# Kernel optimization log

Hardware: AMD Instinct MI355X
Metric: run time of the kernel (lower is better)

## Reference

```python
import jax, jax.numpy as jnp
import numpy as np

N_NODES = 50000
N_FEAT = 128
N_HIDDEN = 256
N_CLASSES = 1
N_EDGES = 800000


def gcn_layer(x, src, dst, W, b, n_nodes):
    """GCNConv: D^-1/2 (A + I) D^-1/2 X W + b, via gather-scatter over edges."""
    h = x @ W  # [N, out]
    # add self loops
    loop = jnp.arange(n_nodes, dtype=src.dtype)
    s = jnp.concatenate([src, loop])
    d = jnp.concatenate([dst, loop])
    deg = jax.ops.segment_sum(jnp.ones_like(d, dtype=h.dtype), d, num_segments=n_nodes)
    inv_sqrt = jax.lax.rsqrt(jnp.maximum(deg, 1.0))
    norm = inv_sqrt[s] * inv_sqrt[d]  # [E+N]
    msgs = h[s] * norm[:, None]       # gather: [E+N, out]
    out = jax.ops.segment_sum(msgs, d, num_segments=n_nodes)  # scatter-add
    return out + b


def setup_inputs() -> dict:
    key = jax.random.key(0)
    k1, k2, k3, k4 = jax.random.split(key, 4)
    x = jax.random.normal(k1, (N_NODES, N_FEAT), dtype=jnp.float32)
    edge_index = jax.random.randint(k2, (2, N_EDGES), 0, N_NODES, dtype=jnp.int32)
    s1 = 1.0 / np.sqrt(N_FEAT)
    s2 = 1.0 / np.sqrt(N_HIDDEN)
    W1 = jax.random.uniform(k3, (N_FEAT, N_HIDDEN), jnp.float32, -s1, s1)
    b1 = jnp.zeros((N_HIDDEN,), jnp.float32)
    W2 = jax.random.uniform(k4, (N_HIDDEN, N_CLASSES), jnp.float32, -s2, s2)
    b2 = jnp.zeros((N_CLASSES,), jnp.float32)
    return {"x": x, "edge_index": edge_index, "W1": W1, "b1": b1, "W2": W2, "b2": b2}


def reference(x, edge_index, W1, b1, W2, b2):
    src, dst = edge_index[0], edge_index[1]
    n = x.shape[0]
    h = gcn_layer(x, src, dst, W1, b1, n)
    h = jax.nn.relu(h)  # dropout=0.0 -> identity
    out = gcn_layer(h, src, dst, W2, b2, n)
    return out  # [N, n_classes]
```

## Files before the change

kernel.cpp:

```cpp
#include <hip/hip_runtime.h>

typedef unsigned int uint;
typedef unsigned short ushort;
typedef __attribute__((ext_vector_type(8))) short short8;
typedef __attribute__((ext_vector_type(4))) float f32x4;

#define CAP  64
#define BM16 16
#define STR  68

__device__ __forceinline__ float bf_lo(uint p) { return __uint_as_float(p << 16); }
__device__ __forceinline__ float bf_hi(uint p) { return __uint_as_float(p & 0xffff0000u); }
__device__ __forceinline__ uint rne_lo(uint u) { return (u + 0x7fffu + ((u >> 16) & 1u)) >> 16; }
__device__ __forceinline__ uint rne_hi(uint u) { return (u + 0x7fffu + ((u >> 16) & 1u)) & 0xffff0000u; }

__global__ void k_bucket(const int* __restrict__ src, const int* __restrict__ dst,
                         int* __restrict__ cnt, ushort* __restrict__ col,
                         const float* __restrict__ W1, uint* __restrict__ wpack, int E) {
  int gid = blockIdx.x * blockDim.x + threadIdx.x;
  if (gid < 4096) {
    int kk = gid >> 10, rem = gid & 1023, ntile = rem >> 6, lane = rem & 63;
    int quad = lane >> 4, nn = ntile * 16 + (lane & 15);
    uint d[4];
#pragma unroll
    for (int jp = 0; jp < 4; ++jp) {
      int k = kk * 32 + quad * 8 + 2 * jp;
      uint lo = rne_lo(__float_as_uint(W1[k * 256 + nn]));
      uint hi = rne_hi(__float_as_uint(W1[(k + 1) * 256 + nn]));
      d[jp] = lo | hi;
    }
    *(uint4*)&wpack[gid * 4] = make_uint4(d[0], d[1], d[2], d[3]);
  } else {
    int e = gid - 4096;
    if (e < E) {
      int d = dst[e];
      int s = src[e];
      int p = atomicAdd(&cnt[d], 1);
      if (p < CAP) col[d * CAP + p] = (ushort)s;
    }
  }
}

__global__ void k_prep2(const float2* __restrict__ x2, const int* __restrict__ cnt,
                        uint* __restrict__ xs, float* __restrict__ inv,
                        int N, int nconv) {
  int gid = blockIdx.x * blockDim.x + threadIdx.x;
  if (gid < N) {
    inv[gid] = rsqrtf((float)(cnt[gid] + 1));
  } else if (gid < N + nconv) {
    int cid = gid - N;
    int node = cid >> 6;
    float invd = rsqrtf((float)(cnt[node] + 1));
    float2 f = x2[cid];
    xs[cid] = rne_lo(__float_as_uint(invd * f.x)) | rne_hi(__float_as_uint(invd * f.y));
  }
}

__global__ __launch_bounds__(256, 2) void k_agg_gemm(
    const uint* __restrict__ xs, const ushort* __restrict__ col,
    const int* __restrict__ cnt, const float* __restrict__ inv,
    const uint* __restrict__ wpack, const float* __restrict__ b1,
    const float* __restrict__ W2, float* __restrict__ cz, int N) {
  __shared__ uint As[BM16 * STR];
  __shared__ float red[64];
  int t = threadIdx.x, wave = t >> 6, lane = t & 63;
  int m0 = blockIdx.x * BM16;

  for (int rr = 0; rr < 4; ++rr) {
    int m = wave * 4 + rr;
    int node = m0 + m;
    float2 acc = make_float2(0.f, 0.f);
    if (node < N) {
      uint pd = xs[(size_t)node * 64 + lane];
      acc.x = bf_lo(pd);
      acc.y = bf_hi(pd);
      int e = min(cnt[node], CAP);
      int ce = (int)col[node * CAP + lane];
      int p = 0;
      for (; p + 15 < e; p += 16) {
        uint pv[16];
#pragma unroll
        for (int j = 0; j < 16; ++j) {
          int s = __shfl(ce, p + j);
          pv[j] = xs[(size_t)s * 64 + lane];
        }
#pragma unroll
        for (int j = 0; j < 16; ++j) {
          acc.x += bf_lo(pv[j]);
          acc.y += bf_hi(pv[j]);
        }
      }
      for (; p + 3 < e; p += 4) {
        uint pv[4];
#pragma unroll
        for (int j = 0; j < 4; ++j) {
          int s = __shfl(ce, p + j);
          pv[j] = xs[(size_t)s * 64 + lane];
        }
#pragma unroll
        for (int j = 0; j < 4; ++j) {
          acc.x += bf_lo(pv[j]);
          acc.y += bf_hi(pv[j]);
        }
      }
      for (; p < e; ++p) {
        int s = __shfl(ce, p);
        uint p0 = xs[(size_t)s * 64 + lane];
        acc.x += bf_lo(p0);
        acc.y += bf_hi(p0);
      }
      float invd = inv[node];
      acc.x *= invd;
      acc.y *= invd;
    }
    As[m * STR + lane] = rne_lo(__float_as_uint(acc.x)) | rne_hi(__float_as_uint(acc.y));
  }
  __syncthreads();

  int quad = lane >> 4, mrow = lane & 15;
  f32x4 acc[4];
#pragma unroll
  for (int nt = 0; nt < 4; ++nt) acc[nt] = (f32x4){0.f, 0.f, 0.f, 0.f};

#pragma unroll
  for (int kk = 0; kk < 4; ++kk) {
    short8 af = *(const short8*)&As[mrow * STR + kk * 16 + quad * 4];
#pragma unroll
    for (int nt = 0; nt < 4; ++nt) {
      int ntile = wave * 4 + nt;
      short8 bf = *(const short8*)&wpack[((kk * 16 + ntile) * 64 + lane) * 4];
      acc[nt] = __builtin_amdgcn_mfma_f32_16x16x32_bf16(af, bf, acc[nt], 0, 0, 0);
    }
  }

  float partial[4] = {0.f, 0.f, 0.f, 0.f};
#pragma unroll
  for (int nt = 0; nt < 4; ++nt) {
    int c = (wave * 4 + nt) * 16 + mrow;
    float b1c = b1[c], w2c = W2[c];
#pragma unroll
    for (int r = 0; r < 4; ++r) {
      float h = fmaxf(acc[nt][r] + b1c, 0.f);
      partial[r] = fmaf(h, w2c, partial[r]);
    }
  }
#pragma unroll
  for (int r = 0; r < 4; ++r) {
    float p = partial[r];
    p += __shfl_xor(p, 1); p += __shfl_xor(p, 2);
    p += __shfl_xor(p, 4); p += __shfl_xor(p, 8);
    if (mrow == 0) red[wave * 16 + quad * 4 + r] = p;
  }
  __syncthreads();
  if (t < 16) {
    int node = m0 + t;
    if (node < N) {
      float s = red[t] + red[16 + t] + red[32 + t] + red[48 + t];
      cz[node] = inv[node] * s;
    }
  }
}

__global__ void k_agg2(const ushort* __restrict__ col, const int* __restrict__ cnt,
                       const float* __restrict__ inv, const float* __restrict__ cz,
                       const float* __restrict__ b2, float* __restrict__ out, int N) {
  int g = blockIdx.x * blockDim.x + threadIdx.x;
  int node = g >> 2, q = g & 3;
  if (node >= N) return;
  int e = min(cnt[node], CAP);
  float acc = (q == 0) ? cz[node] : 0.f;
  const ushort* cp = &col[node * CAP];
  for (int p = q; p < e; p += 4) acc += cz[cp[p]];
  acc += __shfl_xor(acc, 1);
  acc += __shfl_xor(acc, 2);
  if (q == 0) out[node] = inv[node] * acc + b2[0];
}

extern "C" void kernel_launch(void* const* d_in, const int* in_sizes, int n_in,
                              void* d_out, int out_size, void* d_ws, size_t ws_size,
                              hipStream_t stream) {
  const float* x  = (const float*)d_in[0];
  const int*   ei = (const int*)d_in[1];
  const float* W1 = (const float*)d_in[2];
  const float* b1 = (const float*)d_in[3];
  const float* W2 = (const float*)d_in[4];
  const float* b2 = (const float*)d_in[5];
  int N = in_sizes[0] / 128;
  int E = in_sizes[1] / 2;
  const int* src = ei;
  const int* dst = ei + E;
  float* out = (float*)d_out;

  char* w = (char*)d_ws;
  size_t o = 0;
  auto carve = [&](size_t bytes) { char* p = w + o; o += (bytes + 255) & ~(size_t)255; return p; };
  int*    cnt   = (int*)   carve((size_t)N * 4);
  ushort* col   = (ushort*)carve((size_t)N * CAP * 2);
  uint*   xs    = (uint*)  carve((size_t)N * 64 * 4);
  float*  inv   = (float*) carve((size_t)N * 4);
  uint*   wpack = (uint*)  carve(16384 * 4);
  float*  cz    = (float*) carve((size_t)N * 4);

  hipMemsetAsync(cnt, 0, (size_t)N * sizeof(int), stream);

  int tbuck = 4096 + E;
  k_bucket<<<(tbuck + 255) / 256, 256, 0, stream>>>(src, dst, cnt, col, W1, wpack, E);

  int nconv = N * 64;
  int tprep = N + nconv;
  k_prep2<<<(tprep + 255) / 256, 256, 0, stream>>>(
      (const float2*)x, cnt, xs, inv, N, nconv);

  k_agg_gemm<<<(N + BM16 - 1) / BM16, 256, 0, stream>>>(
      xs, col, cnt, inv, wpack, b1, W2, cz, N);

  long long tot2 = (long long)N * 4;
  k_agg2<<<(int)((tot2 + 255) / 256), 256, 0, stream>>>(col, cnt, inv, cz, b2, out, N);
}
```

Before: 174.0 us.

## Merge bucketing and bf16 conversion into one kernel, apply source norm in gather

Bucketing of edges by destination, W1 packing and the bf16 conversion of x now run concurrently in one kernel with disjoint block groups, so the separate prep launch disappears. Because x is no longer pre-scaled by the degree norm, the conversion no longer depends on the bucketing counts. The aggregation kernel instead reads each neighbour's count, computes its rsqrt and applies it with an FMA during the gather. Bucketing blocks each own one of eight destination slices, which localises the atomics but makes every such block scan the full edge list. The extra per-edge count lookup and rsqrt, and the eightfold edge reads, add cost in exchange for one fewer launch and no inv buffer.

```diff
diff --git a/kernel.cpp b/kernel.cpp
--- a/kernel.cpp
+++ b/kernel.cpp
@@ -5,62 +5,64 @@
 typedef __attribute__((ext_vector_type(8))) short short8;
 typedef __attribute__((ext_vector_type(4))) float f32x4;
 
-#define CAP  64
-#define BM16 16
-#define STR  68
+#define CAP   64
+#define BM16  16
+#define STR   68
+#define NB_B  256
+#define NB_C  256
 
 __device__ __forceinline__ float bf_lo(uint p) { return __uint_as_float(p << 16); }
 __device__ __forceinline__ float bf_hi(uint p) { return __uint_as_float(p & 0xffff0000u); }
 __device__ __forceinline__ uint rne_lo(uint u) { return (u + 0x7fffu + ((u >> 16) & 1u)) >> 16; }
 __device__ __forceinline__ uint rne_hi(uint u) { return (u + 0x7fffu + ((u >> 16) & 1u)) & 0xffff0000u; }
 
-__global__ void k_bucket(const int* __restrict__ src, const int* __restrict__ dst,
-                         int* __restrict__ cnt, ushort* __restrict__ col,
-                         const float* __restrict__ W1, uint* __restrict__ wpack, int E) {
-  int gid = blockIdx.x * blockDim.x + threadIdx.x;
-  if (gid < 4096) {
-    int kk = gid >> 10, rem = gid & 1023, ntile = rem >> 6, lane = rem & 63;
-    int quad = lane >> 4, nn = ntile * 16 + (lane & 15);
-    uint d[4];
-#pragma unroll
-    for (int jp = 0; jp < 4; ++jp) {
-      int k = kk * 32 + quad * 8 + 2 * jp;
-      uint lo = rne_lo(__float_as_uint(W1[k * 256 + nn]));
-      uint hi = rne_hi(__float_as_uint(W1[(k + 1) * 256 + nn]));
-      d[jp] = lo | hi;
-    }
-    *(uint4*)&wpack[gid * 4] = make_uint4(d[0], d[1], d[2], d[3]);
+__global__ void k_bucket_conv(const int* __restrict__ src, const int* __restrict__ dst,
+                              int* __restrict__ cnt, ushort* __restrict__ col,
+                              const float2* __restrict__ x2, uint* __restrict__ xs,
+                              const float* __restrict__ W1, uint* __restrict__ wpack,
+                              int N, int E, int nconv) {
+  int t = threadIdx.x;
+  if (blockIdx.x < NB_B) {
+    int slice = blockIdx.x & 7;
+    int bid = blockIdx.x >> 3;
+    int S = (N + 7) / 8;
+    int lo = slice * S, hi = min(N, lo + S);
+    for (int e = bid * 256 + t; e < E; e += (NB_B / 8) * 256) {
+      int d = dst[e];
+      if (d >= lo && d < hi) {
+        int p = atomicAdd(&cnt[d], 1);
+        if (p < CAP) col[d * CAP + p] = (ushort)src[e];
+      }
+    }
   } else {
-    int e = gid - 4096;
-    if (e < E) {
-      int d = dst[e];
-      int s = src[e];
-      int p = atomicAdd(&cnt[d], 1);
-      if (p < CAP) col[d * CAP + p] = (ushort)s;
-    }
-  }
-}
-
-__global__ void k_prep2(const float2* __restrict__ x2, const int* __restrict__ cnt,
-                        uint* __restrict__ xs, float* __restrict__ inv,
-                        int N, int nconv) {
-  int gid = blockIdx.x * blockDim.x + threadIdx.x;
-  if (gid < N) {
-    inv[gid] = rsqrtf((float)(cnt[gid] + 1));
-  } else if (gid < N + nconv) {
-    int cid = gid - N;
-    int node = cid >> 6;
-    float invd = rsqrtf((float)(cnt[node] + 1));
-    float2 f = x2[cid];
-    xs[cid] = rne_lo(__float_as_uint(invd * f.x)) | rne_hi(__float_as_uint(invd * f.y));
+    int tot = 4096 + nconv;
+    for (int g = (blockIdx.x - NB_B) * 256 + t; g < tot; g += NB_C * 256) {
+      if (g < 4096) {
+        int kk = g >> 10, rem = g & 1023, ntile = rem >> 6, ln = rem & 63;
+        int quad = ln >> 4, nn = ntile * 16 + (ln & 15);
+        uint d[4];
+#pragma unroll
+        for (int jp = 0; jp < 4; ++jp) {
+          int k = kk * 32 + quad * 8 + 2 * jp;
+          uint lov = rne_lo(__float_as_uint(W1[k * 256 + nn]));
+          uint hiv = rne_hi(__float_as_uint(W1[(k + 1) * 256 + nn]));
+          d[jp] = lov | hiv;
+        }
+        *(uint4*)&wpack[g * 4] = make_uint4(d[0], d[1], d[2], d[3]);
+      } else {
+        int cid = g - 4096;
+        float2 f = x2[cid];
+        xs[cid] = rne_lo(__float_as_uint(f.x)) | rne_hi(__float_as_uint(f.y));
+      }
+    }
   }
 }
 
 __global__ __launch_bounds__(256, 2) void k_agg_gemm(
     const uint* __restrict__ xs, const ushort* __restrict__ col,
-    const int* __restrict__ cnt, const float* __restrict__ inv,
-    const uint* __restrict__ wpack, const float* __restrict__ b1,
-    const float* __restrict__ W2, float* __restrict__ cz, int N) {
+    const int* __restrict__ cnt, const uint* __restrict__ wpack,
+    const float* __restrict__ b1, const float* __restrict__ W2,
+    float* __restrict__ cz, int N) {
   __shared__ uint As[BM16 * STR];
   __shared__ float red[64];
   int t = threadIdx.x, wave = t >> 6, lane = t & 63;
@@ -71,45 +73,49 @@
     int node = m0 + m;
     float2 acc = make_float2(0.f, 0.f);
     if (node < N) {
+      float invd = rsqrtf((float)(cnt[node] + 1));
       uint pd = xs[(size_t)node * 64 + lane];
-      acc.x = bf_lo(pd);
-      acc.y = bf_hi(pd);
+      acc.x = invd * bf_lo(pd);
+      acc.y = invd * bf_hi(pd);
       int e = min(cnt[node], CAP);
       int ce = (int)col[node * CAP + lane];
+      float cw = rsqrtf((float)(cnt[ce] + 1));
       int p = 0;
       for (; p + 15 < e; p += 16) {
-        uint pv[16];
+        uint pv[16]; float cv[16];
 #pragma unroll
         for (int j = 0; j < 16; ++j) {
           int s = __shfl(ce, p + j);
+          cv[j] = __shfl(cw, p + j);
           pv[j] = xs[(size_t)s * 64 + lane];
         }
 #pragma unroll
         for (int j = 0; j < 16; ++j) {
-          acc.x += bf_lo(pv[j]);
-          acc.y += bf_hi(pv[j]);
+          acc.x = fmaf(bf_lo(pv[j]), cv[j], acc.x);
+          acc.y = fmaf(bf_hi(pv[j]), cv[j], acc.y);
         }
       }
       for (; p + 3 < e; p += 4) {
-        uint pv[4];
+        uint pv[4]; float cv[4];
 #pragma unroll
         for (int j = 0; j < 4; ++j) {
           int s = __shfl(ce, p + j);
+          cv[j] = __shfl(cw, p + j);
           pv[j] = xs[(size_t)s * 64 + lane];
         }
 #pragma unroll
         for (int j = 0; j < 4; ++j) {
-          acc.x += bf_lo(pv[j]);
-          acc.y += bf_hi(pv[j]);
+          acc.x = fmaf(bf_lo(pv[j]), cv[j], acc.x);
+          acc.y = fmaf(bf_hi(pv[j]), cv[j], acc.y);
         }
       }
       for (; p < e; ++p) {
         int s = __shfl(ce, p);
+        float c = __shfl(cw, p);
         uint p0 = xs[(size_t)s * 64 + lane];
-        acc.x += bf_lo(p0);
-        acc.y += bf_hi(p0);
-      }
-      float invd = inv[node];
+        acc.x = fmaf(bf_lo(p0), c, acc.x);
+        acc.y = fmaf(bf_hi(p0), c, acc.y);
+      }
       acc.x *= invd;
       acc.y *= invd;
     }
@@ -121,7 +127,6 @@
   f32x4 acc[4];
 #pragma unroll
   for (int nt = 0; nt < 4; ++nt) acc[nt] = (f32x4){0.f, 0.f, 0.f, 0.f};
-
 #pragma unroll
   for (int kk = 0; kk < 4; ++kk) {
     short8 af = *(const short8*)&As[mrow * STR + kk * 16 + quad * 4];
@@ -156,14 +161,14 @@
     int node = m0 + t;
     if (node < N) {
       float s = red[t] + red[16 + t] + red[32 + t] + red[48 + t];
-      cz[node] = inv[node] * s;
+      cz[node] = rsqrtf((float)(cnt[node] + 1)) * s;
     }
   }
 }
 
 __global__ void k_agg2(const ushort* __restrict__ col, const int* __restrict__ cnt,
-                       const float* __restrict__ inv, const float* __restrict__ cz,
-                       const float* __restrict__ b2, float* __restrict__ out, int N) {
+                       const float* __restrict__ cz, const float* __restrict__ b2,
+                       float* __restrict__ out, int N) {
   int g = blockIdx.x * blockDim.x + threadIdx.x;
   int node = g >> 2, q = g & 3;
   if (node >= N) return;
@@ -173,18 +178,18 @@
   for (int p = q; p < e; p += 4) acc += cz[cp[p]];
   acc += __shfl_xor(acc, 1);
   acc += __shfl_xor(acc, 2);
-  if (q == 0) out[node] = inv[node] * acc + b2[0];
+  if (q == 0) out[node] = rsqrtf((float)(cnt[node] + 1)) * acc + b2[0];
 }
 
 extern "C" void kernel_launch(void* const* d_in, const int* in_sizes, int n_in,
                               void* d_out, int out_size, void* d_ws, size_t ws_size,
                               hipStream_t stream) {
-  const float* x  = (const float*)d_in[0];
-  const int*   ei = (const int*)d_in[1];
-  const float* W1 = (const float*)d_in[2];
-  const float* b1 = (const float*)d_in[3];
-  const float* W2 = (const float*)d_in[4];
-  const float* b2 = (const float*)d_in[5];
+  const float2* x2 = (const float2*)d_in[0];
+  const int*    ei = (const int*)d_in[1];
+  const float*  W1 = (const float*)d_in[2];
+  const float*  b1 = (const float*)d_in[3];
+  const float*  W2 = (const float*)d_in[4];
+  const float*  b2 = (const float*)d_in[5];
   int N = in_sizes[0] / 128;
   int E = in_sizes[1] / 2;
   const int* src = ei;
@@ -197,23 +202,18 @@
   int*    cnt   = (int*)   carve((size_t)N * 4);
   ushort* col   = (ushort*)carve((size_t)N * CAP * 2);
   uint*   xs    = (uint*)  carve((size_t)N * 64 * 4);
-  float*  inv   = (float*) carve((size_t)N * 4);
   uint*   wpack = (uint*)  carve(16384 * 4);
   float*  cz    = (float*) carve((size_t)N * 4);
 
   hipMemsetAsync(cnt, 0, (size_t)N * sizeof(int), stream);
 
-  int tbuck = 4096 + E;
-  k_bucket<<<(tbuck + 255) / 256, 256, 0, stream>>>(src, dst, cnt, col, W1, wpack, E);
-
   int nconv = N * 64;
-  int tprep = N + nconv;
-  k_prep2<<<(tprep + 255) / 256, 256, 0, stream>>>(
-      (const float2*)x, cnt, xs, inv, N, nconv);
+  k_bucket_conv<<<NB_B + NB_C, 256, 0, stream>>>(
+      src, dst, cnt, col, x2, xs, W1, wpack, N, E, nconv);
 
   k_agg_gemm<<<(N + BM16 - 1) / BM16, 256, 0, stream>>>(
-      xs, col, cnt, inv, wpack, b1, W2, cz, N);
+      xs, col, cnt, wpack, b1, W2, cz, N);
 
   long long tot2 = (long long)N * 4;
-  k_agg2<<<(int)((tot2 + 255) / 256), 256, 0, stream>>>(col, cnt, inv, cz, b2, out, N);
-}
+  k_agg2<<<(int)((tot2 + 255) / 256), 256, 0, stream>>>(col, cnt, cz, b2, out, N);
+}
```

Result: slower. 217.6 us (+25.1%).
